# Kernel tuning notes

Measured on AMD Instinct MI355X. Metric: run time of the kernel, lower is better.

Reference implementation:

```python
import jax, jax.numpy as jnp
import numpy as np

N, C_IN, C_OUT, H = 4096, 1024, 512, 4
D = C_OUT // H  # per-head output dim
TEMP = 1.0


def setup_inputs() -> dict:
    key = jax.random.key(0)
    ks = jax.random.split(key, 6)
    node_feats = jax.random.normal(ks[0], (N, C_IN), dtype=jnp.float32)
    # sparse 0/1 adjacency mask, avg degree ~ 0.02*N
    adj_matrix = jax.random.bernoulli(ks[1], 0.02, (N, N)).astype(jnp.float32)
    lim_w = np.sqrt(6.0 / (C_IN + D))
    lim_v = np.sqrt(6.0 / (D + 1))
    W = jax.random.uniform(ks[2], (H, C_IN, D), jnp.float32, -lim_w, lim_w)
    b = jnp.zeros((H, D), dtype=jnp.float32)
    v0 = jax.random.uniform(ks[3], (H, D), jnp.float32, -lim_v, lim_v)
    v1 = jax.random.uniform(ks[4], (H, D), jnp.float32, -lim_v, lim_v)
    return {"node_feats": node_feats, "adj_matrix": adj_matrix,
            "W": W, "b": b, "v0": v0, "v1": v1}


def reference(node_feats, adj_matrix, W, b, v0, v1):
    # per-head linear projection: [H, N, D]
    h = jnp.einsum('nc,hcd->hnd', node_feats, W) + b[:, None, :]
    f1 = jnp.einsum('hnd,hd->hn', h, v0)  # [H, N]
    f2 = jnp.einsum('hnd,hd->hn', h, v1)  # [H, N]
    logits = adj_matrix[None, :, :] * (f1[:, :, None] + f2[:, None, :])
    # torch to_sparse drops exact zeros; sparse.softmax normalizes over
    # the remaining (nonzero) entries only, zeros stay zero when densified.
    mask = logits != 0
    vals = (jax.nn.sigmoid(logits) - 0.5) / TEMP
    rowmax = jnp.max(jnp.where(mask, vals, -1e30), axis=-1, keepdims=True)
    e = jnp.where(mask, jnp.exp(vals - rowmax), 0.0)
    denom = jnp.sum(e, axis=-1, keepdims=True)
    p = jnp.where(denom > 0, e / jnp.maximum(denom, 1e-30), 0.0)
    out = jnp.einsum('hnm,hmd->hnd', p, h)  # [H, N, D]
    # concat heads along feature dim -> [N, H*D]
    return out.transpose(1, 0, 2).reshape(node_feats.shape[0], -1)
```

## Files before the change

### kernel.cpp

```cpp
#include <hip/hip_runtime.h>
#include <hip/hip_bf16.h>

#define N_NODES 4096
#define C_IN    1024
#define H_HEADS 4
#define D_HEAD  128
#define C_OUT   512
#define DEG_CAP 256
#define PRE_ROWS 1024

typedef __attribute__((ext_vector_type(8))) short short8;
typedef __attribute__((ext_vector_type(4))) float f32x4;

__device__ __forceinline__ unsigned short f2bf(float f) {
    unsigned u = __float_as_uint(f);
    u += 0x7FFFu + ((u >> 16) & 1u);
    return (unsigned short)(u >> 16);
}
__device__ __forceinline__ float bf2f(unsigned short u) {
    return __uint_as_float((unsigned)u << 16);
}
__device__ __forceinline__ float sigv(float s) {
    return 1.f / (1.f + __expf(-s)) - 0.5f;
}

#define GLOAD_LDS16(gp, lp)                                                        \
    __builtin_amdgcn_global_load_lds(                                              \
        (const __attribute__((address_space(1))) unsigned int*)(gp),               \
        (__attribute__((address_space(3))) unsigned int*)(lp), 16, 0, 0)

__device__ __forceinline__ void scan_row(int i, const float* __restrict__ adj,
                                         unsigned short* __restrict__ idx,
                                         int* __restrict__ nnz, int* wtot,
                                         int t, int lane, int wid) {
    const float4* arow = (const float4*)(adj + (size_t)i * N_NODES);
    float4 av[4];
#pragma unroll
    for (int r = 0; r < 4; ++r) av[r] = arow[r * 256 + t];

    int cnt = 0;
#pragma unroll
    for (int r = 0; r < 4; ++r)
        cnt += (av[r].x != 0.f) + (av[r].y != 0.f) + (av[r].z != 0.f) + (av[r].w != 0.f);
    int v = cnt;
#pragma unroll
    for (int off = 1; off < 64; off <<= 1) {
        int u = __shfl_up(v, off);
        if (lane >= off) v += u;
    }
    if (lane == 63) wtot[wid] = v;
    __syncthreads();
    int wpre = 0, total = 0;
#pragma unroll
    for (int w = 0; w < 4; ++w) {
        int tw = wtot[w];
        if (w < wid) wpre += tw;
        total += tw;
    }
    int off = wpre + v - cnt;
    unsigned short* ir = idx + (size_t)i * DEG_CAP;
#pragma unroll
    for (int r = 0; r < 4; ++r) {
        int j0 = (r * 256 + t) * 4;
        if (av[r].x != 0.f) { if (off < DEG_CAP) ir[off] = (unsigned short)j0;       off++; }
        if (av[r].y != 0.f) { if (off < DEG_CAP) ir[off] = (unsigned short)(j0 + 1); off++; }
        if (av[r].z != 0.f) { if (off < DEG_CAP) ir[off] = (unsigned short)(j0 + 2); off++; }
        if (av[r].w != 0.f) { if (off < DEG_CAP) ir[off] = (unsigned short)(j0 + 3); off++; }
    }
    if (t == 0) nnz[i] = min(total, DEG_CAP);
}

__global__ void k_pre(const float* __restrict__ X, const float* __restrict__ W,
                      const float* __restrict__ adj,
                      unsigned short* __restrict__ Xb, unsigned short* __restrict__ Wt,
                      float* __restrict__ F12,
                      unsigned short* __restrict__ idx, int* __restrict__ nnz) {
    __shared__ int wtot[4];
    const int t    = threadIdx.x;
    const int lane = t & 63;
    const int wid  = t >> 6;
    const int bid  = blockIdx.x;

    if (bid < 2048) {
        size_t g = (size_t)bid * 256 + t;
        const float4* s = (const float4*)(X + g * 8);
        float4 a = s[0], b2 = s[1];
        ushort4 p0, p1;
        p0.x = f2bf(a.x);  p0.y = f2bf(a.y);  p0.z = f2bf(a.z);  p0.w = f2bf(a.w);
        p1.x = f2bf(b2.x); p1.y = f2bf(b2.y); p1.z = f2bf(b2.z); p1.w = f2bf(b2.w);
        ushort4* d = (ushort4*)(Xb + g * 8);
        d[0] = p0; d[1] = p1;
    } else if (bid < 2560) {
        int g = (bid - 2048) * 256 + t;
        int o = g * 4;
        int c  = o & 1023;
        int hd = o >> 10;
        int dd = hd & 127;
        int h  = hd >> 7;
        const float* src = W + (size_t)h * C_IN * D_HEAD + (size_t)c * D_HEAD + dd;
        ushort4 p;
        p.x = f2bf(src[0 * D_HEAD]);
        p.y = f2bf(src[1 * D_HEAD]);
        p.z = f2bf(src[2 * D_HEAD]);
        p.w = f2bf(src[3 * D_HEAD]);
        *(ushort4*)(Wt + o) = p;
    } else if (bid < 2592) {
        int z = (bid - 2560) * 256 + t;
        *(f32x4*)(F12 + (size_t)z * 4) = (f32x4){0.f, 0.f, 0.f, 0.f};
    } else {
        scan_row(bid - 2592, adj, idx, nnz, wtot, t, lane, wid);
    }
}

__global__ void k_work(const unsigned short* __restrict__ Xb,
                       const unsigned short* __restrict__ Wt,
                       const float* __restrict__ bias,
                       const float* __restrict__ v0, const float* __restrict__ v1,
                       const float* __restrict__ adj,
                       unsigned short* __restrict__ Hb,
                       float* __restrict__ F1, float* __restrict__ F2,
                       unsigned short* __restrict__ idx, int* __restrict__ nnz) {
    __shared__ __align__(16) unsigned char smem[32768];
    const int t    = threadIdx.x;
    const int lane = t & 63;
    const int wid  = t >> 6;

    if (blockIdx.x < 512) {
        unsigned short* ldsA = (unsigned short*)smem;
        unsigned short* ldsB = ldsA + 2 * 64 * 64;
        const int wrow = wid >> 1, wcol = wid & 1;
        const int bid  = blockIdx.x;
        const int lin  = (bid & 7) * 64 + (bid >> 3);
        const int rowStart = (lin >> 3) * 64;
        const int colStart = (lin & 7) * 64;

        f32x4 acc[2][2];
#pragma unroll
        for (int m = 0; m < 2; ++m)
#pragma unroll
            for (int n = 0; n < 2; ++n) acc[m][n] = (f32x4){0.f, 0.f, 0.f, 0.f};

        const int lrow = lane >> 2;
        const int lkq  = (lane & 3) ^ ((lane >> 3) & 3);

        auto stage = [&](int buf, int k0) {
#pragma unroll
            for (int ii = 0; ii < 2; ++ii) {
                int c  = wid * 2 + ii;
                int h  = c >> 2, rb = c & 3;
                const unsigned short* g =
                    Xb + (size_t)(rowStart + rb * 16 + lrow) * C_IN + k0 + h * 32 + lkq * 8;
                GLOAD_LDS16(g, ldsA + buf * 4096 + h * 2048 + rb * 512);
            }
#pragma unroll
            for (int ii = 0; ii < 2; ++ii) {
                int c  = wid * 2 + ii;
                int h  = c >> 2, db = c & 3;
                const unsigned short* g =
                    Wt + (size_t)(colStart + db * 16 + lrow) * C_IN + k0 + h * 32 + lkq * 8;
                GLOAD_LDS16(g, ldsB + buf * 4096 + h * 2048 + db * 512);
            }
        };

        stage(0, 0);
        __syncthreads();

        const int fr = lane & 15;
        const int sw = ((lane >> 4) ^ ((fr >> 1) & 3)) * 8;
        int cur = 0;
        for (int kt = 0; kt < 16; ++kt) {
            if (kt < 15) stage(cur ^ 1, (kt + 1) * 64);
            const unsigned short* __restrict__ lA = ldsA + cur * 4096;
            const unsigned short* __restrict__ lB = ldsB + cur * 4096;
#pragma unroll
            for (int h = 0; h < 2; ++h) {
                short8 bfr[2];
#pragma unroll
                for (int n = 0; n < 2; ++n)
                    bfr[n] = *(const short8*)(lB + h * 2048 + (wcol * 32 + n * 16 + fr) * 32 + sw);
#pragma unroll
                for (int m = 0; m < 2; ++m) {
                    short8 a = *(const short8*)(lA + h * 2048 + (wrow * 32 + m * 16 + fr) * 32 + sw);
#pragma unroll
                    for (int n = 0; n < 2; ++n)
                        acc[m][n] = __builtin_amdgcn_mfma_f32_16x16x32_bf16(a, bfr[n], acc[m][n], 0, 0, 0);
                }
            }
            __syncthreads();
            cur ^= 1;
        }

        const int c0 = colStart + wcol * 32 + (lane & 15);
        const int c1 = c0 + 16;
        const int head = c0 >> 7;
        const float bb0 = bias[c0], bb1 = bias[c1];
        const float v0c0 = v0[c0], v0c1 = v0[c1];
        const float v1c0 = v1[c0], v1c1 = v1[c1];
#pragma unroll
        for (int m = 0; m < 2; ++m) {
            int row_g = rowStart + wrow * 32 + m * 16 + (lane >> 4) * 4;
#pragma unroll
            for (int r = 0; r < 4; ++r) {
                float h0 = acc[m][0][r] + bb0;
                float h1 = acc[m][1][r] + bb1;
                Hb[(size_t)(row_g + r) * C_OUT + c0] = f2bf(h0);
                Hb[(size_t)(row_g + r) * C_OUT + c1] = f2bf(h1);
                float p1 = h0 * v0c0 + h1 * v0c1;
                float p2 = h0 * v1c0 + h1 * v1c1;
#pragma unroll
                for (int off = 8; off; off >>= 1) {
                    p1 += __shfl_xor(p1, off);
                    p2 += __shfl_xor(p2, off);
                }
                if ((lane & 15) == 0) {
                    atomicAdd(&F1[(row_g + r) * 4 + head], p1);
                    atomicAdd(&F2[(row_g + r) * 4 + head], p2);
                }
            }
        }
    } else {
        scan_row(blockIdx.x - 512 + PRE_ROWS, adj, idx, nnz, (int*)smem, t, lane, wid);
    }
}

__global__ void k_pv(const unsigned short* __restrict__ idx, const int* __restrict__ nnz,
                     const float* __restrict__ F1, const float* __restrict__ F2,
                     const unsigned short* __restrict__ Hb, float* __restrict__ Out) {
    __shared__ unsigned short jl[DEG_CAP];
    __shared__ float ev[H_HEADS][DEG_CAP];

    const int i    = blockIdx.x;
    const int t    = threadIdx.x;
    const int lane = t & 63;
    const int w    = t >> 6;

    const int nv = nnz[i];

    ushort4 jv = *(const ushort4*)(idx + (size_t)i * DEG_CAP + 4 * lane);
    *(ushort4*)(jl + 4 * lane) = jv;

    const float f1h = F1[i * 4 + w];
    float dsum = 0.f;
#pragma unroll
    for (int s = 0; s < 4; ++s) {
        int e = lane + 64 * s;
        float ee = 0.f;
        if (e < nv) {
            int j = jl[e];
            float sg = f1h + F2[j * 4 + w];
            ee = (sg != 0.f) ? __expf(sigv(sg)) : 0.f;
        }
        ev[w][e] = ee;
        dsum += ee;
    }
#pragma unroll
    for (int o2 = 32; o2; o2 >>= 1) dsum += __shfl_xor(dsum, o2);

    const unsigned short* __restrict__ hp = Hb + (size_t)w * D_HEAD + 2 * lane;
    float a0 = 0.f, a1 = 0.f, b0 = 0.f, b1 = 0.f;
    int jj = 0;
#pragma unroll 4
    for (; jj + 1 < nv; jj += 2) {
        int ja = jl[jj], jb = jl[jj + 1];
        float ea = ev[w][jj], eb = ev[w][jj + 1];
        unsigned pa = *(const unsigned*)(hp + (size_t)ja * C_OUT);
        unsigned pb = *(const unsigned*)(hp + (size_t)jb * C_OUT);
        a0 += ea * bf2f((unsigned short)(pa & 0xFFFFu));
        a1 += ea * bf2f((unsigned short)(pa >> 16));
        b0 += eb * bf2f((unsigned short)(pb & 0xFFFFu));
        b1 += eb * bf2f((unsigned short)(pb >> 16));
    }
    if (jj < nv) {
        int ja = jl[jj];
        float ea = ev[w][jj];
        unsigned pa = *(const unsigned*)(hp + (size_t)ja * C_OUT);
        a0 += ea * bf2f((unsigned short)(pa & 0xFFFFu));
        a1 += ea * bf2f((unsigned short)(pa >> 16));
    }

    float2 o;
    if (dsum > 0.f) {
        float inv = 1.f / fmaxf(dsum, 1e-30f);
        o.x = (a0 + b0) * inv;
        o.y = (a1 + b1) * inv;
    } else {
        o.x = 0.f; o.y = 0.f;
    }
    *(float2*)(Out + (size_t)i * C_OUT + w * D_HEAD + 2 * lane) = o;
}

extern "C" void kernel_launch(void* const* d_in, const int* in_sizes, int n_in,
                              void* d_out, int out_size, void* d_ws, size_t ws_size,
                              hipStream_t stream) {
    const float* X   = (const float*)d_in[0];
    const float* adj = (const float*)d_in[1];
    const float* W   = (const float*)d_in[2];
    const float* b   = (const float*)d_in[3];
    const float* v0  = (const float*)d_in[4];
    const float* v1  = (const float*)d_in[5];
    float* out = (float*)d_out;

    char* ws = (char*)d_ws;
    unsigned short* Wt  = (unsigned short*)ws;
    unsigned short* Xb  = (unsigned short*)(ws + (size_t)1 * 1024 * 1024);
    unsigned short* Hb  = (unsigned short*)(ws + (size_t)9 * 1024 * 1024);
    float*          F1  = (float*)(ws + (size_t)13 * 1024 * 1024);
    float*          F2  = F1 + N_NODES * 4;
    unsigned short* idx = (unsigned short*)(ws + (size_t)14 * 1024 * 1024);
    int*            nnz = (int*)(ws + (size_t)16 * 1024 * 1024);

    k_pre<<<2592 + PRE_ROWS, 256, 0, stream>>>(X, W, adj, Xb, Wt, F1, idx, nnz);
    k_work<<<512 + (N_NODES - PRE_ROWS), 256, 0, stream>>>(Xb, Wt, b, v0, v1, adj,
                                                           Hb, F1, F2, idx, nnz);
    k_pv<<<N_NODES, 256, 0, stream>>>(idx, nnz, F1, F2, Hb, out);
}
```

Baseline: 60.36 us.

## Fuse X bf16 conversion into GEMM staging and move all adjacency scanning to k_work

The separate pass that converts X from fp32 to bf16 is removed. The GEMM now loads fp32 X tiles straight into LDS through a swizzled layout and converts them to bf16 in registers before each MFMA. All adjacency row scans move out of the first kernel into the second, and the GEMM's LDS double buffering is replaced by a single buffer with a sync after every load. The aim is to avoid writing and re-reading the bf16 copy of X and to shrink the first kernel, at the cost of fetching twice the A bytes per tile, doing the conversion inside the GEMM loop, and losing the overlap between loads and compute.

```diff
diff --git a/kernel.cpp b/kernel.cpp
--- a/kernel.cpp
+++ b/kernel.cpp
@@ -7,7 +7,6 @@
 #define D_HEAD  128
 #define C_OUT   512
 #define DEG_CAP 256
-#define PRE_ROWS 1024
 
 typedef __attribute__((ext_vector_type(8))) short short8;
 typedef __attribute__((ext_vector_type(4))) float f32x4;
@@ -70,28 +69,12 @@
     if (t == 0) nnz[i] = min(total, DEG_CAP);
 }
 
-__global__ void k_pre(const float* __restrict__ X, const float* __restrict__ W,
-                      const float* __restrict__ adj,
-                      unsigned short* __restrict__ Xb, unsigned short* __restrict__ Wt,
-                      float* __restrict__ F12,
-                      unsigned short* __restrict__ idx, int* __restrict__ nnz) {
-    __shared__ int wtot[4];
-    const int t    = threadIdx.x;
-    const int lane = t & 63;
-    const int wid  = t >> 6;
-    const int bid  = blockIdx.x;
-
-    if (bid < 2048) {
-        size_t g = (size_t)bid * 256 + t;
-        const float4* s = (const float4*)(X + g * 8);
-        float4 a = s[0], b2 = s[1];
-        ushort4 p0, p1;
-        p0.x = f2bf(a.x);  p0.y = f2bf(a.y);  p0.z = f2bf(a.z);  p0.w = f2bf(a.w);
-        p1.x = f2bf(b2.x); p1.y = f2bf(b2.y); p1.z = f2bf(b2.z); p1.w = f2bf(b2.w);
-        ushort4* d = (ushort4*)(Xb + g * 8);
-        d[0] = p0; d[1] = p1;
-    } else if (bid < 2560) {
-        int g = (bid - 2048) * 256 + t;
+__global__ void k_pre(const float* __restrict__ W, unsigned short* __restrict__ Wt,
+                      float* __restrict__ F12) {
+    const int t   = threadIdx.x;
+    const int bid = blockIdx.x;
+    if (bid < 512) {
+        int g = bid * 256 + t;
         int o = g * 4;
         int c  = o & 1023;
         int hd = o >> 10;
@@ -104,15 +87,13 @@
         p.z = f2bf(src[2 * D_HEAD]);
         p.w = f2bf(src[3 * D_HEAD]);
         *(ushort4*)(Wt + o) = p;
-    } else if (bid < 2592) {
-        int z = (bid - 2560) * 256 + t;
+    } else {
+        int z = (bid - 512) * 256 + t;
         *(f32x4*)(F12 + (size_t)z * 4) = (f32x4){0.f, 0.f, 0.f, 0.f};
-    } else {
-        scan_row(bid - 2592, adj, idx, nnz, wtot, t, lane, wid);
-    }
-}
-
-__global__ void k_work(const unsigned short* __restrict__ Xb,
+    }
+}
+
+__global__ void k_work(const float* __restrict__ X,
                        const unsigned short* __restrict__ Wt,
                        const float* __restrict__ bias,
                        const float* __restrict__ v0, const float* __restrict__ v1,
@@ -120,14 +101,14 @@
                        unsigned short* __restrict__ Hb,
                        float* __restrict__ F1, float* __restrict__ F2,
                        unsigned short* __restrict__ idx, int* __restrict__ nnz) {
-    __shared__ __align__(16) unsigned char smem[32768];
+    __shared__ __align__(16) unsigned char smem[24576];
     const int t    = threadIdx.x;
     const int lane = t & 63;
     const int wid  = t >> 6;
 
     if (blockIdx.x < 512) {
-        unsigned short* ldsA = (unsigned short*)smem;
-        unsigned short* ldsB = ldsA + 2 * 64 * 64;
+        float*          ldsAf = (float*)smem;
+        unsigned short* ldsB  = (unsigned short*)(smem + 16384);
         const int wrow = wid >> 1, wcol = wid & 1;
         const int bid  = blockIdx.x;
         const int lin  = (bid & 7) * 64 + (bid >> 3);
@@ -142,15 +123,22 @@
 
         const int lrow = lane >> 2;
         const int lkq  = (lane & 3) ^ ((lane >> 3) & 3);
-
-        auto stage = [&](int buf, int k0) {
-#pragma unroll
-            for (int ii = 0; ii < 2; ++ii) {
-                int c  = wid * 2 + ii;
-                int h  = c >> 2, rb = c & 3;
-                const unsigned short* g =
-                    Xb + (size_t)(rowStart + rb * 16 + lrow) * C_IN + k0 + h * 32 + lkq * 8;
-                GLOAD_LDS16(g, ldsA + buf * 4096 + h * 2048 + rb * 512);
+        const int arow4 = lane >> 4;
+        const int aslot = lane & 15;
+
+        const int fr = lane & 63 & 15;
+        const int sw = ((lane >> 4) ^ ((fr >> 1) & 3)) * 8;
+        const int ko = lane >> 4;
+
+        for (int kt = 0; kt < 16; ++kt) {
+            const int k0 = kt * 64;
+#pragma unroll
+            for (int ii = 0; ii < 4; ++ii) {
+                int c   = wid * 4 + ii;
+                int row = 4 * c + arow4;
+                int q   = aslot ^ (4 * (c & 1) + arow4);
+                const float* g = X + (size_t)(rowStart + row) * C_IN + k0 + q * 4;
+                GLOAD_LDS16(g, ldsAf + c * 256);
             }
 #pragma unroll
             for (int ii = 0; ii < 2; ++ii) {
@@ -158,36 +146,33 @@
                 int h  = c >> 2, db = c & 3;
                 const unsigned short* g =
                     Wt + (size_t)(colStart + db * 16 + lrow) * C_IN + k0 + h * 32 + lkq * 8;
-                GLOAD_LDS16(g, ldsB + buf * 4096 + h * 2048 + db * 512);
+                GLOAD_LDS16(g, ldsB + h * 2048 + db * 512);
             }
-        };
-
-        stage(0, 0);
-        __syncthreads();
-
-        const int fr = lane & 15;
-        const int sw = ((lane >> 4) ^ ((fr >> 1) & 3)) * 8;
-        int cur = 0;
-        for (int kt = 0; kt < 16; ++kt) {
-            if (kt < 15) stage(cur ^ 1, (kt + 1) * 64);
-            const unsigned short* __restrict__ lA = ldsA + cur * 4096;
-            const unsigned short* __restrict__ lB = ldsB + cur * 4096;
+            __syncthreads();
+
 #pragma unroll
             for (int h = 0; h < 2; ++h) {
                 short8 bfr[2];
 #pragma unroll
                 for (int n = 0; n < 2; ++n)
-                    bfr[n] = *(const short8*)(lB + h * 2048 + (wcol * 32 + n * 16 + fr) * 32 + sw);
+                    bfr[n] = *(const short8*)(ldsB + h * 2048 + (wcol * 32 + n * 16 + fr) * 32 + sw);
 #pragma unroll
                 for (int m = 0; m < 2; ++m) {
-                    short8 a = *(const short8*)(lA + h * 2048 + (wrow * 32 + m * 16 + fr) * 32 + sw);
+                    int row = wrow * 32 + m * 16 + fr;
+                    int qr0 = h * 8 + ko * 2;
+                    float4 x0 = *(const float4*)(ldsAf + row * 64 + ((qr0 ^ (fr & 7)) << 2));
+                    float4 x1 = *(const float4*)(ldsAf + row * 64 + (((qr0 + 1) ^ (fr & 7)) << 2));
+                    short8 af;
+                    af[0] = (short)f2bf(x0.x); af[1] = (short)f2bf(x0.y);
+                    af[2] = (short)f2bf(x0.z); af[3] = (short)f2bf(x0.w);
+                    af[4] = (short)f2bf(x1.x); af[5] = (short)f2bf(x1.y);
+                    af[6] = (short)f2bf(x1.z); af[7] = (short)f2bf(x1.w);
 #pragma unroll
                     for (int n = 0; n < 2; ++n)
-                        acc[m][n] = __builtin_amdgcn_mfma_f32_16x16x32_bf16(a, bfr[n], acc[m][n], 0, 0, 0);
+                        acc[m][n] = __builtin_amdgcn_mfma_f32_16x16x32_bf16(af, bfr[n], acc[m][n], 0, 0, 0);
                 }
             }
             __syncthreads();
-            cur ^= 1;
         }
 
         const int c0 = colStart + wcol * 32 + (lane & 15);
@@ -219,7 +204,7 @@
             }
         }
     } else {
-        scan_row(blockIdx.x - 512 + PRE_ROWS, adj, idx, nnz, (int*)smem, t, lane, wid);
+        scan_row(blockIdx.x - 512, adj, idx, nnz, (int*)smem, t, lane, wid);
     }
 }
 
@@ -302,15 +287,14 @@
 
     char* ws = (char*)d_ws;
     unsigned short* Wt  = (unsigned short*)ws;
-    unsigned short* Xb  = (unsigned short*)(ws + (size_t)1 * 1024 * 1024);
-    unsigned short* Hb  = (unsigned short*)(ws + (size_t)9 * 1024 * 1024);
-    float*          F1  = (float*)(ws + (size_t)13 * 1024 * 1024);
+    unsigned short* Hb  = (unsigned short*)(ws + (size_t)1 * 1024 * 1024);
+    float*          F1  = (float*)(ws + (size_t)5 * 1024 * 1024);
     float*          F2  = F1 + N_NODES * 4;
-    unsigned short* idx = (unsigned short*)(ws + (size_t)14 * 1024 * 1024);
-    int*            nnz = (int*)(ws + (size_t)16 * 1024 * 1024);
-
-    k_pre<<<2592 + PRE_ROWS, 256, 0, stream>>>(X, W, adj, Xb, Wt, F1, idx, nnz);
-    k_work<<<512 + (N_NODES - PRE_ROWS), 256, 0, stream>>>(Xb, Wt, b, v0, v1, adj,
-                                                           Hb, F1, F2, idx, nnz);
+    unsigned short* idx = (unsigned short*)(ws + (size_t)6 * 1024 * 1024);
+    int*            nnz = (int*)(ws + (size_t)8 * 1024 * 1024);
+
+    k_pre<<<544, 256, 0, stream>>>(W, Wt, F1);
+    k_work<<<512 + N_NODES, 256, 0, stream>>>(X, Wt, b, v0, v1, adj,
+                                              Hb, F1, F2, idx, nnz);
     k_pv<<<N_NODES, 256, 0, stream>>>(idx, nnz, F1, F2, Hb, out);
 }
```

New measurement: 59.76 us. About the same (-1.0%).

## Use ballot-based row compaction and move all adjacency scans into GEMM kernel

Applied to the files above, without the earlier changes.

Rewrites the adjacency row scan to compact nonzero indices with wave ballots and popcounts, replacing the shuffle-based prefix scan and per-element branching. All adjacency rows are now scanned by extra blocks in the GEMM kernel rather than split with the conversion kernel. The first kernel becomes a pure bf16 conversion kernel. This rebalances work across kernels so the memory-bound scan overlaps the projection GEMM, at the cost of more scalar loads per lane.

```diff
diff --git a/kernel.cpp b/kernel.cpp
--- a/kernel.cpp
+++ b/kernel.cpp
@@ -7,7 +7,6 @@
 #define D_HEAD  128
 #define C_OUT   512
 #define DEG_CAP 256
-#define PRE_ROWS 1024
 
 typedef __attribute__((ext_vector_type(8))) short short8;
 typedef __attribute__((ext_vector_type(4))) float f32x4;
@@ -33,54 +32,45 @@
                                          unsigned short* __restrict__ idx,
                                          int* __restrict__ nnz, int* wtot,
                                          int t, int lane, int wid) {
-    const float4* arow = (const float4*)(adj + (size_t)i * N_NODES);
-    float4 av[4];
-#pragma unroll
-    for (int r = 0; r < 4; ++r) av[r] = arow[r * 256 + t];
-
+    const float* arow = adj + (size_t)i * N_NODES + wid * 1024;
+    unsigned long long masks[16];
     int cnt = 0;
 #pragma unroll
-    for (int r = 0; r < 4; ++r)
-        cnt += (av[r].x != 0.f) + (av[r].y != 0.f) + (av[r].z != 0.f) + (av[r].w != 0.f);
-    int v = cnt;
-#pragma unroll
-    for (int off = 1; off < 64; off <<= 1) {
-        int u = __shfl_up(v, off);
-        if (lane >= off) v += u;
-    }
-    if (lane == 63) wtot[wid] = v;
+    for (int s = 0; s < 16; ++s) {
+        float a = arow[s * 64 + lane];
+        unsigned long long m = __ballot(a != 0.f);
+        masks[s] = m;
+        cnt += __popcll(m);
+    }
+    if (lane == 0) wtot[wid] = cnt;
     __syncthreads();
-    int wpre = 0, total = 0;
+    int base = 0, total = 0;
 #pragma unroll
     for (int w = 0; w < 4; ++w) {
         int tw = wtot[w];
-        if (w < wid) wpre += tw;
+        if (w < wid) base += tw;
         total += tw;
     }
-    int off = wpre + v - cnt;
     unsigned short* ir = idx + (size_t)i * DEG_CAP;
-#pragma unroll
-    for (int r = 0; r < 4; ++r) {
-        int j0 = (r * 256 + t) * 4;
-        if (av[r].x != 0.f) { if (off < DEG_CAP) ir[off] = (unsigned short)j0;       off++; }
-        if (av[r].y != 0.f) { if (off < DEG_CAP) ir[off] = (unsigned short)(j0 + 1); off++; }
-        if (av[r].z != 0.f) { if (off < DEG_CAP) ir[off] = (unsigned short)(j0 + 2); off++; }
-        if (av[r].w != 0.f) { if (off < DEG_CAP) ir[off] = (unsigned short)(j0 + 3); off++; }
+    const unsigned long long below = (lane == 63) ? 0x7FFFFFFFFFFFFFFFull
+                                                  : ((1ull << lane) - 1ull);
+#pragma unroll
+    for (int s = 0; s < 16; ++s) {
+        unsigned long long m = masks[s];
+        if ((m >> lane) & 1ull) {
+            int off = base + __popcll(m & below);
+            if (off < DEG_CAP) ir[off] = (unsigned short)(wid * 1024 + s * 64 + lane);
+        }
+        base += __popcll(m);
     }
     if (t == 0) nnz[i] = min(total, DEG_CAP);
 }
 
-__global__ void k_pre(const float* __restrict__ X, const float* __restrict__ W,
-                      const float* __restrict__ adj,
+__global__ void k_cvt(const float* __restrict__ X, const float* __restrict__ W,
                       unsigned short* __restrict__ Xb, unsigned short* __restrict__ Wt,
-                      float* __restrict__ F12,
-                      unsigned short* __restrict__ idx, int* __restrict__ nnz) {
-    __shared__ int wtot[4];
-    const int t    = threadIdx.x;
-    const int lane = t & 63;
-    const int wid  = t >> 6;
-    const int bid  = blockIdx.x;
-
+                      float* __restrict__ F12) {
+    const int t   = threadIdx.x;
+    const int bid = blockIdx.x;
     if (bid < 2048) {
         size_t g = (size_t)bid * 256 + t;
         const float4* s = (const float4*)(X + g * 8);
@@ -104,11 +94,9 @@
         p.z = f2bf(src[2 * D_HEAD]);
         p.w = f2bf(src[3 * D_HEAD]);
         *(ushort4*)(Wt + o) = p;
-    } else if (bid < 2592) {
+    } else {
         int z = (bid - 2560) * 256 + t;
         *(f32x4*)(F12 + (size_t)z * 4) = (f32x4){0.f, 0.f, 0.f, 0.f};
-    } else {
-        scan_row(bid - 2592, adj, idx, nnz, wtot, t, lane, wid);
     }
 }
 
@@ -219,7 +207,7 @@
             }
         }
     } else {
-        scan_row(blockIdx.x - 512 + PRE_ROWS, adj, idx, nnz, (int*)smem, t, lane, wid);
+        scan_row(blockIdx.x - 512, adj, idx, nnz, (int*)smem, t, lane, wid);
     }
 }
 
@@ -309,8 +297,8 @@
     unsigned short* idx = (unsigned short*)(ws + (size_t)14 * 1024 * 1024);
     int*            nnz = (int*)(ws + (size_t)16 * 1024 * 1024);
 
-    k_pre<<<2592 + PRE_ROWS, 256, 0, stream>>>(X, W, adj, Xb, Wt, F1, idx, nnz);
-    k_work<<<512 + (N_NODES - PRE_ROWS), 256, 0, stream>>>(Xb, Wt, b, v0, v1, adj,
-                                                           Hb, F1, F2, idx, nnz);
+    k_cvt<<<2592, 256, 0, stream>>>(X, W, Xb, Wt, F1);
+    k_work<<<512 + N_NODES, 256, 0, stream>>>(Xb, Wt, b, v0, v1, adj,
+                                              Hb, F1, F2, idx, nnz);
     k_pv<<<N_NODES, 256, 0, stream>>>(idx, nnz, F1, F2, Hb, out);
 }
```

After: 60.60 us. Within noise of the previous version (+0.4%).
